# Kernel optimization log

Hardware: AMD Instinct MI355X
Metric: run time of the kernel (lower is better)

Reference implementation:

```python
import jax, jax.numpy as jnp
import numpy as np

DIM = 1024
NUM_HEADS = 16
HEAD_DIM = DIM // NUM_HEADS
SCALE = HEAD_DIM ** -0.5


def setup_inputs() -> dict:
    key = jax.random.key(0)
    ks = jax.random.split(key, 11)
    B, N, M = 8, 1024, 1024
    s = DIM ** -0.5  # init scale for weights
    return {
        "x": jax.random.normal(ks[0], (B, N, DIM), jnp.float32),
        "context": jax.random.normal(ks[1], (B, M, DIM), jnp.float32),
        "Wq": jax.random.normal(ks[2], (DIM, DIM), jnp.float32) * s,
        "bq": jax.random.normal(ks[3], (DIM,), jnp.float32) * 0.01,
        "Wk": jax.random.normal(ks[4], (DIM, DIM), jnp.float32) * s,
        "bk": jax.random.normal(ks[5], (DIM,), jnp.float32) * 0.01,
        "Wv": jax.random.normal(ks[6], (DIM, DIM), jnp.float32) * s,
        "bv": jax.random.normal(ks[7], (DIM,), jnp.float32) * 0.01,
        "Wo": jax.random.normal(ks[8], (DIM, DIM), jnp.float32) * s,
        "bo": jax.random.normal(ks[9], (DIM,), jnp.float32) * 0.01,
    }


def reference(x, context, Wq, bq, Wk, bk, Wv, bv, Wo, bo):
    B, N, _ = x.shape
    M = context.shape[1]
    # Linear projections (torch Linear: x @ W.T + b; here W stored as [in, out])
    q = x @ Wq + bq            # [B, N, DIM]
    k = context @ Wk + bk      # [B, M, DIM]
    v = context @ Wv + bv      # [B, M, DIM]
    # split heads: b n (h d) -> b h n d
    q = q.reshape(B, N, NUM_HEADS, HEAD_DIM).transpose(0, 2, 1, 3)
    k = k.reshape(B, M, NUM_HEADS, HEAD_DIM).transpose(0, 2, 1, 3)
    v = v.reshape(B, M, NUM_HEADS, HEAD_DIM).transpose(0, 2, 1, 3)
    dots = jnp.einsum('bhnd,bhmd->bhnm', q, k) * SCALE
    attn = jax.nn.softmax(dots, axis=-1)
    out = jnp.einsum('bhnm,bhmd->bhnd', attn, v)   # [B, H, N, d]
    out = out.transpose(0, 2, 1, 3).reshape(B, N, DIM)  # b h n d -> b n (h d)
    return out @ Wo + bo
```

## Files before the change

### kernel.cpp

```cpp
#include <hip/hip_runtime.h>

typedef unsigned short u16;
typedef __attribute__((ext_vector_type(8))) short bf16x8;
typedef __attribute__((ext_vector_type(4))) float f32x4;
typedef __attribute__((ext_vector_type(16))) float f32x16;
typedef __attribute__((ext_vector_type(4))) unsigned u32x4;

#define MFMA16 __builtin_amdgcn_mfma_f32_16x16x32_bf16
#define MFMA32 __builtin_amdgcn_mfma_f32_32x32x16_bf16

__device__ __forceinline__ u16 f2b(float f) {
  unsigned u = __builtin_bit_cast(unsigned, f);
  u = (u + 0x7fffu + ((u >> 16) & 1u)) >> 16;
  return (u16)u;
}

__device__ __forceinline__ void gload_lds16(const u16* g, u16* l) {
  __builtin_amdgcn_global_load_lds((const __attribute__((address_space(1))) void*)g,
                                   (__attribute__((address_space(3))) void*)l, 16, 0, 0);
}

__global__ void cvt_bf16(const float* __restrict__ a, const float* __restrict__ b,
                         u16* __restrict__ oa, u16* __restrict__ ob, int n4) {
  int i = blockIdx.x * blockDim.x + threadIdx.x;
  if (i >= n4) return;
  const float* in = blockIdx.z ? b : a;
  u16* out = blockIdx.z ? ob : oa;
  float4 v = reinterpret_cast<const float4*>(in)[i];
  ushort4 o = make_ushort4(f2b(v.x), f2b(v.y), f2b(v.z), f2b(v.w));
  reinterpret_cast<ushort4*>(out)[i] = o;
}

__global__ void wtrans(const float* __restrict__ w0, const float* __restrict__ w1,
                       const float* __restrict__ w2, const float* __restrict__ w3,
                       u16* __restrict__ o0, u16* __restrict__ o1,
                       u16* __restrict__ o2, u16* __restrict__ o3) {
  const float* src = blockIdx.z == 0 ? w0 : blockIdx.z == 1 ? w1 : blockIdx.z == 2 ? w2 : w3;
  u16* dst = blockIdx.z == 0 ? o0 : blockIdx.z == 1 ? o1 : blockIdx.z == 2 ? o2 : o3;
  __shared__ float t[64][65];
  const int tid = threadIdx.x;
  const int r0 = blockIdx.y * 64, c0 = blockIdx.x * 64;
  #pragma unroll
  for (int it = 0; it < 4; ++it) {
    int row = it * 16 + (tid >> 4);
    int col = (tid & 15) * 4;
    float4 v = *reinterpret_cast<const float4*>(&src[(size_t)(r0 + row) * 1024 + c0 + col]);
    t[row][col] = v.x; t[row][col + 1] = v.y; t[row][col + 2] = v.z; t[row][col + 3] = v.w;
  }
  __syncthreads();
  #pragma unroll
  for (int it = 0; it < 2; ++it) {
    int c = it * 32 + (tid >> 3);
    int r8 = (tid & 7) * 8;
    u16 tmp[8];
    #pragma unroll
    for (int k = 0; k < 8; ++k) tmp[k] = f2b(t[r8 + k][c]);
    uint4 pk;
    pk.x = (unsigned)tmp[0] | ((unsigned)tmp[1] << 16);
    pk.y = (unsigned)tmp[2] | ((unsigned)tmp[3] << 16);
    pk.z = (unsigned)tmp[4] | ((unsigned)tmp[5] << 16);
    pk.w = (unsigned)tmp[6] | ((unsigned)tmp[7] << 16);
    *reinterpret_cast<uint4*>(&dst[(size_t)(c0 + c) * 1024 + r0 + r8]) = pk;
  }
}

__device__ __forceinline__ void gemm_core(const u16* __restrict__ A, const u16* __restrict__ Wt,
                                          f32x4 (&acc)[4][4], int brow, int bcol,
                                          u16* __restrict__ smem) {
  const int tid = threadIdx.x;
  const int lane = tid & 63;
  const int w = tid >> 6;
  const int wr = w >> 1, wc = w & 1;
  const int l16 = lane & 15, g = lane >> 4;

  auto stage = [&](int buf, int kt) {
    #pragma unroll
    for (int it = 0; it < 4; ++it) {
      int c = it * 256 + tid;
      int row = (c >> 2) & 127;
      int ks = c >> 9;
      int k8 = c & 3;
      const size_t gofs = (size_t)kt * 64 + ks * 32 + k8 * 8;
      gload_lds16(&A[(size_t)(brow + row) * 1024 + gofs],
                  &smem[buf * 8192 + (it * 256 + w * 64) * 8]);
      gload_lds16(&Wt[(size_t)(bcol + row) * 1024 + gofs],
                  &smem[16384 + buf * 8192 + (it * 256 + w * 64) * 8]);
    }
  };

  stage(0, 0);
  __syncthreads();
  int cur = 0;
  for (int kt = 0; kt < 16; ++kt) {
    if (kt < 15) stage(cur ^ 1, kt + 1);
    const u16* As = &smem[cur * 8192];
    const u16* Bs = &smem[16384 + cur * 8192];
    #pragma unroll
    for (int ks = 0; ks < 2; ++ks) {
      bf16x8 a[4], b[4];
      const int kb = ks * 4096 + g * 8;
      #pragma unroll
      for (int mi = 0; mi < 4; ++mi)
        a[mi] = *reinterpret_cast<const bf16x8*>(&As[kb + (wr * 64 + mi * 16 + l16) * 32]);
      #pragma unroll
      for (int ni = 0; ni < 4; ++ni)
        b[ni] = *reinterpret_cast<const bf16x8*>(&Bs[kb + (wc * 64 + ni * 16 + l16) * 32]);
      #pragma unroll
      for (int mi = 0; mi < 4; ++mi)
        #pragma unroll
        for (int ni = 0; ni < 4; ++ni)
          acc[mi][ni] = MFMA16(a[mi], b[ni], acc[mi][ni], 0, 0, 0);
    }
    __syncthreads();
    cur ^= 1;
  }
}

__global__ __launch_bounds__(256, 2) void gemm_qkv(const u16* __restrict__ xb, const u16* __restrict__ cb,
                                                   const u16* __restrict__ Wqt, const u16* __restrict__ Wkt,
                                                   const u16* __restrict__ Wvt,
                                                   const float* __restrict__ bq, const float* __restrict__ bk,
                                                   const float* __restrict__ bv,
                                                   u16* __restrict__ Qb, u16* __restrict__ Kb,
                                                   u16* __restrict__ Vt) {
  __shared__ u16 smem[32768];
  const int z = blockIdx.z;
  const u16* A = z == 0 ? xb : cb;
  const u16* W = z == 0 ? Wqt : z == 1 ? Wkt : Wvt;
  const float* bias = z == 0 ? bq : z == 1 ? bk : bv;
  const int brow = blockIdx.x * 128, bcol = blockIdx.y * 128;
  f32x4 acc[4][4] = {};
  gemm_core(A, W, acc, brow, bcol, smem);

  const int lane = threadIdx.x & 63;
  const int w = threadIdx.x >> 6;
  const int wr = w >> 1, wc = w & 1;
  const int l16 = lane & 15, g = lane >> 4;
  const float CS = 0.125f * 1.44269504089f;

  if (z < 2) {
    u16* o = z == 0 ? Qb : Kb;
    #pragma unroll
    for (int ni = 0; ni < 4; ++ni) {
      const int col = bcol + wc * 64 + ni * 16 + l16;
      const float bz = bias[col];
      #pragma unroll
      for (int mi = 0; mi < 4; ++mi) {
        const int r0 = brow + wr * 64 + mi * 16 + g * 4;
        f32x4 v = acc[mi][ni];
        #pragma unroll
        for (int j = 0; j < 4; ++j) {
          float val = v[j] + bz;
          if (z == 0) val *= CS;
          o[(size_t)(r0 + j) * 1024 + col] = f2b(val);
        }
      }
    }
  } else {
    u16* T = &smem[w * 4608];
    #pragma unroll
    for (int ni = 0; ni < 4; ++ni) {
      const int col = bcol + wc * 64 + ni * 16 + l16;
      const float bz = bias[col];
      #pragma unroll
      for (int mi = 0; mi < 4; ++mi) {
        f32x4 v = acc[mi][ni];
        #pragma unroll
        for (int j = 0; j < 4; ++j)
          T[(ni * 16 + l16) * 72 + mi * 16 + g * 4 + j] = f2b(v[j] + bz);
      }
    }
    const int h = (bcol + wc * 64) >> 6;
    const int m0 = brow + wr * 64;
    const int bb = m0 >> 10, mloc = m0 & 1023;
    u16* vb = &Vt[((size_t)(bb * 16 + h) * 64) * 1024 + mloc];
    #pragma unroll
    for (int it = 0; it < 8; ++it) {
      const int d = it * 8 + (lane >> 3);
      const int m8 = (lane & 7) * 8;
      bf16x8 val = *reinterpret_cast<const bf16x8*>(&T[d * 72 + m8]);
      *reinterpret_cast<bf16x8*>(&vb[(size_t)d * 1024 + m8]) = val;
    }
  }
}

__global__ __launch_bounds__(256, 2) void gemm_o(const u16* __restrict__ A, const u16* __restrict__ Wt,
                                                 const float* __restrict__ bias, float* __restrict__ outp) {
  __shared__ u16 smem[32768];
  const int brow = blockIdx.x * 128, bcol = blockIdx.y * 128;
  f32x4 acc[4][4] = {};
  gemm_core(A, Wt, acc, brow, bcol, smem);
  const int lane = threadIdx.x & 63;
  const int w = threadIdx.x >> 6;
  const int wr = w >> 1, wc = w & 1;
  const int l16 = lane & 15, g = lane >> 4;
  #pragma unroll
  for (int ni = 0; ni < 4; ++ni) {
    const int col = bcol + wc * 64 + ni * 16 + l16;
    const float bz = bias[col];
    #pragma unroll
    for (int mi = 0; mi < 4; ++mi) {
      const int r0 = brow + wr * 64 + mi * 16 + g * 4;
      f32x4 v = acc[mi][ni];
      #pragma unroll
      for (int j = 0; j < 4; ++j) outp[(size_t)(r0 + j) * 1024 + col] = v[j] + bz;
    }
  }
}

__global__ __launch_bounds__(256, 2) void attn2(const u16* __restrict__ Q, const u16* __restrict__ K,
                                                const u16* __restrict__ Vt, u16* __restrict__ AO) {
  __shared__ u16 Ks[2][64 * 64];
  __shared__ u16 Vs[2][64 * 64];
  const int tid = threadIdx.x, lane = tid & 63, w = tid >> 6;
  const int l32 = lane & 31, u = lane >> 5;
  const int id = blockIdx.x;
  const int v = (id & 7) * 128 + (id >> 3);
  const int qt = v & 7, h = (v >> 3) & 15, b = v >> 7;
  const int q0 = qt * 128 + w * 32;
  const int sw = l32 & 7;

  bf16x8 qf[4];
  {
    const u16* qp = &Q[(size_t)(b * 1024 + q0 + l32) * 1024 + h * 64 + u * 8];
    #pragma unroll
    for (int m = 0; m < 4; ++m) qf[m] = *reinterpret_cast<const bf16x8*>(qp + m * 16);
  }

  f32x16 o0 = {}, o1 = {};
  float lr = 0.f;

  const u16* Kg = K + (size_t)(b * 1024) * 1024 + h * 64;
  const u16* Vg = Vt + (size_t)(b * 16 + h) * 64 * 1024;

  auto stage = [&](int buf, int kt) {
    #pragma unroll
    for (int i = 0; i < 2; ++i) {
      int c = w * 128 + i * 64 + lane;
      int r = c >> 3;
      int gc = ((c & 7) ^ (r & 7)) * 8;
      gload_lds16(&Kg[(size_t)(kt * 64 + r) * 1024 + gc], &Ks[buf][(w * 128 + i * 64) * 8]);
      gload_lds16(&Vg[(size_t)r * 1024 + kt * 64 + gc], &Vs[buf][(w * 128 + i * 64) * 8]);
    }
  };

  stage(0, 0);
  __syncthreads();
  int cur = 0;

  for (int kt = 0; kt < 16; ++kt) {
    if (kt < 15) stage(cur ^ 1, kt + 1);

    f32x16 s0 = {}, s1 = {};
    __builtin_amdgcn_s_setprio(1);
    #pragma unroll
    for (int m = 0; m < 4; ++m) {
      bf16x8 k0 = *reinterpret_cast<const bf16x8*>(&Ks[cur][(size_t)l32 * 64 + (((2 * m + u) ^ sw) * 8)]);
      bf16x8 k1 = *reinterpret_cast<const bf16x8*>(&Ks[cur][(size_t)(32 + l32) * 64 + (((2 * m + u) ^ sw) * 8)]);
      s0 = MFMA32(k0, qf[m], s0, 0, 0, 0);
      s1 = MFMA32(k1, qf[m], s1, 0, 0, 0);
    }
    __builtin_amdgcn_s_setprio(0);

    unsigned W0[8], W1[8];
    #pragma unroll
    for (int j = 0; j < 8; ++j) {
      const int r = 4 * (j >> 1) + 2 * (j & 1);
      float pa0 = __builtin_amdgcn_exp2f(s0[r]);
      float pb0 = __builtin_amdgcn_exp2f(s0[r + 1]);
      float pa1 = __builtin_amdgcn_exp2f(s1[r]);
      float pb1 = __builtin_amdgcn_exp2f(s1[r + 1]);
      lr += (pa0 + pb0) + (pa1 + pb1);
      asm("v_cvt_pk_bf16_f32 %0, %1, %2" : "=v"(W0[j]) : "v"(pa0), "v"(pb0));
      asm("v_cvt_pk_bf16_f32 %0, %1, %2" : "=v"(W1[j]) : "v"(pa1), "v"(pb1));
    }

    unsigned paw[4][4];
    #pragma unroll
    for (int ks = 0; ks < 4; ++ks) {
      const int ksl = ks & 1;
      #pragma unroll
      for (int p = 0; p < 2; ++p) {
        unsigned x = (ks < 2) ? W0[4 * ksl + p] : W1[4 * ksl + p];
        unsigned y = (ks < 2) ? W0[4 * ksl + 2 + p] : W1[4 * ksl + 2 + p];
        asm("v_permlane32_swap_b32 %0, %1" : "+v"(x), "+v"(y));
        paw[ks][p] = x;
        paw[ks][2 + p] = y;
      }
    }

    __builtin_amdgcn_s_setprio(1);
    #pragma unroll
    for (int ks = 0; ks < 4; ++ks) {
      bf16x8 pa = __builtin_bit_cast(bf16x8, u32x4{paw[ks][0], paw[ks][1], paw[ks][2], paw[ks][3]});
      bf16x8 v0 = *reinterpret_cast<const bf16x8*>(&Vs[cur][(size_t)l32 * 64 + (((2 * ks + u) ^ sw) * 8)]);
      bf16x8 v1 = *reinterpret_cast<const bf16x8*>(&Vs[cur][(size_t)(32 + l32) * 64 + (((2 * ks + u) ^ sw) * 8)]);
      o0 = MFMA32(pa, v0, o0, 0, 0, 0);
      o1 = MFMA32(pa, v1, o1, 0, 0, 0);
    }
    __builtin_amdgcn_s_setprio(0);

    __syncthreads();
    cur ^= 1;
  }

  float sum = lr + __shfl_xor(lr, 32);
  float rinv = 1.0f / sum;
  u16* aop = &AO[(size_t)(b * 1024 + q0) * 1024 + h * 64 + l32];
  #pragma unroll
  for (int r = 0; r < 16; ++r) {
    const int ql = (r & 3) + 8 * (r >> 2) + 4 * u;
    int ri_i = __builtin_amdgcn_ds_bpermute((ql + (u << 5)) << 2, __builtin_bit_cast(int, rinv));
    float ri = __builtin_bit_cast(float, ri_i);
    aop[(size_t)ql * 1024] = f2b(o0[r] * ri);
    aop[(size_t)ql * 1024 + 32] = f2b(o1[r] * ri);
  }
}

extern "C" void kernel_launch(void* const* d_in, const int* in_sizes, int n_in,
                              void* d_out, int out_size, void* d_ws, size_t ws_size,
                              hipStream_t stream) {
  const float* x   = (const float*)d_in[0];
  const float* ctx = (const float*)d_in[1];
  const float* Wq  = (const float*)d_in[2];
  const float* bq  = (const float*)d_in[3];
  const float* Wk  = (const float*)d_in[4];
  const float* bk  = (const float*)d_in[5];
  const float* Wv  = (const float*)d_in[6];
  const float* bv  = (const float*)d_in[7];
  const float* Wo  = (const float*)d_in[8];
  const float* bo  = (const float*)d_in[9];
  float* out = (float*)d_out;
  char* ws = (char*)d_ws;

  u16* xb  = (u16*)(ws + (size_t)0);
  u16* cb  = (u16*)(ws + ((size_t)16 << 20));
  u16* Qb  = (u16*)(ws + ((size_t)32 << 20));
  u16* Kb  = (u16*)(ws + ((size_t)48 << 20));
  u16* Vt  = (u16*)(ws + ((size_t)64 << 20));
  u16* Wqt = (u16*)(ws + ((size_t)80 << 20));
  u16* Wkt = (u16*)(ws + ((size_t)82 << 20));
  u16* Wvt = (u16*)(ws + ((size_t)84 << 20));
  u16* Wot = (u16*)(ws + ((size_t)86 << 20));

  const int n4 = (8 * 1024 * 1024) / 4;
  cvt_bf16<<<dim3(8192, 1, 2), 256, 0, stream>>>(x, ctx, xb, cb, n4);
  wtrans<<<dim3(16, 16, 4), 256, 0, stream>>>(Wq, Wk, Wv, Wo, Wqt, Wkt, Wvt, Wot);

  gemm_qkv<<<dim3(64, 8, 3), 256, 0, stream>>>(xb, cb, Wqt, Wkt, Wvt, bq, bk, bv, Qb, Kb, Vt);
  attn2<<<dim3(1024), 256, 0, stream>>>(Qb, Kb, Vt, xb );
  gemm_o<<<dim3(64, 8), 256, 0, stream>>>(xb, Wot, bo, out);
}
```

Baseline: 152.4 us.

## Pre-tile K/V into MFMA fragment order and merge prep kernels

The QKV GEMM epilogue now stages results through LDS and writes K and V as contiguous per-(batch,head,64-key) tiles already arranged in MFMA fragment order. Q stores become vectorized 16-byte rows. The attention kernel can then load each tile with contiguous global-to-LDS copies and read fragments with linear, unswizzled LDS addresses. The fp32→bf16 input conversion and weight transpose kernels are merged into one launch, which adds many idle blocks in the weight branch and risks LDS bank conflicts from the new unswizzled reads.

```diff
diff --git a/kernel.cpp b/kernel.cpp
--- a/kernel.cpp
+++ b/kernel.cpp
@@ -20,26 +20,29 @@
                                    (__attribute__((address_space(3))) void*)l, 16, 0, 0);
 }
 
-__global__ void cvt_bf16(const float* __restrict__ a, const float* __restrict__ b,
-                         u16* __restrict__ oa, u16* __restrict__ ob, int n4) {
-  int i = blockIdx.x * blockDim.x + threadIdx.x;
-  if (i >= n4) return;
-  const float* in = blockIdx.z ? b : a;
-  u16* out = blockIdx.z ? ob : oa;
-  float4 v = reinterpret_cast<const float4*>(in)[i];
-  ushort4 o = make_ushort4(f2b(v.x), f2b(v.y), f2b(v.z), f2b(v.w));
-  reinterpret_cast<ushort4*>(out)[i] = o;
-}
-
-__global__ void wtrans(const float* __restrict__ w0, const float* __restrict__ w1,
-                       const float* __restrict__ w2, const float* __restrict__ w3,
-                       u16* __restrict__ o0, u16* __restrict__ o1,
-                       u16* __restrict__ o2, u16* __restrict__ o3) {
-  const float* src = blockIdx.z == 0 ? w0 : blockIdx.z == 1 ? w1 : blockIdx.z == 2 ? w2 : w3;
-  u16* dst = blockIdx.z == 0 ? o0 : blockIdx.z == 1 ? o1 : blockIdx.z == 2 ? o2 : o3;
+__global__ void prep(const float* __restrict__ x, const float* __restrict__ ctx,
+                     u16* __restrict__ xb, u16* __restrict__ cb,
+                     const float* __restrict__ w0, const float* __restrict__ w1,
+                     const float* __restrict__ w2, const float* __restrict__ w3,
+                     u16* __restrict__ o0, u16* __restrict__ o1,
+                     u16* __restrict__ o2, u16* __restrict__ o3) {
   __shared__ float t[64][65];
+  const int z = blockIdx.z;
   const int tid = threadIdx.x;
-  const int r0 = blockIdx.y * 64, c0 = blockIdx.x * 64;
+  if (z < 2) {
+    int i = blockIdx.x * blockDim.x + tid;
+    const float* in = z ? ctx : x;
+    u16* out = z ? cb : xb;
+    float4 v = reinterpret_cast<const float4*>(in)[i];
+    reinterpret_cast<ushort4*>(out)[i] = make_ushort4(f2b(v.x), f2b(v.y), f2b(v.z), f2b(v.w));
+    return;
+  }
+  const int id = blockIdx.x;
+  if (id >= 1024) return;
+  const int wsel = id >> 8;
+  const float* src = wsel == 0 ? w0 : wsel == 1 ? w1 : wsel == 2 ? w2 : w3;
+  u16* dst = wsel == 0 ? o0 : wsel == 1 ? o1 : wsel == 2 ? o2 : o3;
+  const int r0 = ((id >> 4) & 15) * 64, c0 = (id & 15) * 64;
   #pragma unroll
   for (int it = 0; it < 4; ++it) {
     int row = it * 16 + (tid >> 4);
@@ -121,8 +124,8 @@
                                                    const u16* __restrict__ Wvt,
                                                    const float* __restrict__ bq, const float* __restrict__ bk,
                                                    const float* __restrict__ bv,
-                                                   u16* __restrict__ Qb, u16* __restrict__ Kb,
-                                                   u16* __restrict__ Vt) {
+                                                   u16* __restrict__ Qb, u16* __restrict__ Kf,
+                                                   u16* __restrict__ Vf) {
   __shared__ u16 smem[32768];
   const int z = blockIdx.z;
   const u16* A = z == 0 ? xb : cb;
@@ -137,49 +140,71 @@
   const int wr = w >> 1, wc = w & 1;
   const int l16 = lane & 15, g = lane >> 4;
   const float CS = 0.125f * 1.44269504089f;
+  u16* T = &smem[w * 5120];
 
   if (z < 2) {
-    u16* o = z == 0 ? Qb : Kb;
     #pragma unroll
     for (int ni = 0; ni < 4; ++ni) {
-      const int col = bcol + wc * 64 + ni * 16 + l16;
-      const float bz = bias[col];
+      const float bz = bias[bcol + wc * 64 + ni * 16 + l16];
       #pragma unroll
       for (int mi = 0; mi < 4; ++mi) {
-        const int r0 = brow + wr * 64 + mi * 16 + g * 4;
         f32x4 v = acc[mi][ni];
         #pragma unroll
         for (int j = 0; j < 4; ++j) {
           float val = v[j] + bz;
           if (z == 0) val *= CS;
-          o[(size_t)(r0 + j) * 1024 + col] = f2b(val);
+          T[(mi * 16 + g * 4 + j) * 80 + ni * 16 + l16] = f2b(val);
         }
       }
     }
+    const int r0b = brow + wr * 64;
+    const int colb = bcol + wc * 64;
+    if (z == 0) {
+      #pragma unroll
+      for (int it = 0; it < 8; ++it) {
+        const int rl = it * 8 + (lane >> 3);
+        const int c8 = (lane & 7) * 8;
+        bf16x8 val = *reinterpret_cast<const bf16x8*>(&T[rl * 80 + c8]);
+        *reinterpret_cast<bf16x8*>(&Qb[(size_t)(r0b + rl) * 1024 + colb + c8]) = val;
+      }
+    } else {
+      const int h = colb >> 6;
+      const int bb = r0b >> 10;
+      const int kt = (r0b & 1023) >> 6;
+      u16* kb2 = &Kf[(((size_t)(bb * 16 + h)) * 16 + kt) * 4096];
+      #pragma unroll
+      for (int it = 0; it < 8; ++it) {
+        const int rl = it * 8 + (lane >> 3);
+        const int c8 = (lane & 7) * 8;
+        bf16x8 val = *reinterpret_cast<const bf16x8*>(&T[rl * 80 + c8]);
+        const int chunk = (c8 >> 4) * 128 + (rl >> 5) * 64 + ((c8 >> 3) & 1) * 32 + (rl & 31);
+        *reinterpret_cast<bf16x8*>(&kb2[chunk * 8]) = val;
+      }
+    }
   } else {
-    u16* T = &smem[w * 4608];
     #pragma unroll
     for (int ni = 0; ni < 4; ++ni) {
-      const int col = bcol + wc * 64 + ni * 16 + l16;
-      const float bz = bias[col];
+      const float bz = bias[bcol + wc * 64 + ni * 16 + l16];
       #pragma unroll
       for (int mi = 0; mi < 4; ++mi) {
         f32x4 v = acc[mi][ni];
         #pragma unroll
         for (int j = 0; j < 4; ++j)
-          T[(ni * 16 + l16) * 72 + mi * 16 + g * 4 + j] = f2b(v[j] + bz);
+          T[(ni * 16 + l16) * 80 + mi * 16 + g * 4 + j] = f2b(v[j] + bz);
       }
     }
     const int h = (bcol + wc * 64) >> 6;
     const int m0 = brow + wr * 64;
-    const int bb = m0 >> 10, mloc = m0 & 1023;
-    u16* vb = &Vt[((size_t)(bb * 16 + h) * 64) * 1024 + mloc];
+    const int bb = m0 >> 10;
+    const int kt = (m0 & 1023) >> 6;
+    u16* vb = &Vf[(((size_t)(bb * 16 + h)) * 16 + kt) * 4096];
     #pragma unroll
     for (int it = 0; it < 8; ++it) {
       const int d = it * 8 + (lane >> 3);
       const int m8 = (lane & 7) * 8;
-      bf16x8 val = *reinterpret_cast<const bf16x8*>(&T[d * 72 + m8]);
-      *reinterpret_cast<bf16x8*>(&vb[(size_t)d * 1024 + m8]) = val;
+      bf16x8 val = *reinterpret_cast<const bf16x8*>(&T[d * 80 + m8]);
+      const int chunk = (m8 >> 4) * 128 + (d >> 5) * 64 + ((m8 >> 3) & 1) * 32 + (d & 31);
+      *reinterpret_cast<bf16x8*>(&vb[chunk * 8]) = val;
     }
   }
 }
@@ -208,8 +233,8 @@
   }
 }
 
-__global__ __launch_bounds__(256, 2) void attn2(const u16* __restrict__ Q, const u16* __restrict__ K,
-                                                const u16* __restrict__ Vt, u16* __restrict__ AO) {
+__global__ __launch_bounds__(256, 2) void attn2(const u16* __restrict__ Q, const u16* __restrict__ Kf,
+                                                const u16* __restrict__ Vf, u16* __restrict__ AO) {
   __shared__ u16 Ks[2][64 * 64];
   __shared__ u16 Vs[2][64 * 64];
   const int tid = threadIdx.x, lane = tid & 63, w = tid >> 6;
@@ -218,7 +243,6 @@
   const int v = (id & 7) * 128 + (id >> 3);
   const int qt = v & 7, h = (v >> 3) & 15, b = v >> 7;
   const int q0 = qt * 128 + w * 32;
-  const int sw = l32 & 7;
 
   bf16x8 qf[4];
   {
@@ -230,17 +254,15 @@
   f32x16 o0 = {}, o1 = {};
   float lr = 0.f;
 
-  const u16* Kg = K + (size_t)(b * 1024) * 1024 + h * 64;
-  const u16* Vg = Vt + (size_t)(b * 16 + h) * 64 * 1024;
+  const u16* Kbh = Kf + (size_t)(b * 16 + h) * 65536;
+  const u16* Vbh = Vf + (size_t)(b * 16 + h) * 65536;
 
   auto stage = [&](int buf, int kt) {
     #pragma unroll
-    for (int i = 0; i < 2; ++i) {
-      int c = w * 128 + i * 64 + lane;
-      int r = c >> 3;
-      int gc = ((c & 7) ^ (r & 7)) * 8;
-      gload_lds16(&Kg[(size_t)(kt * 64 + r) * 1024 + gc], &Ks[buf][(w * 128 + i * 64) * 8]);
-      gload_lds16(&Vg[(size_t)r * 1024 + kt * 64 + gc], &Vs[buf][(w * 128 + i * 64) * 8]);
+    for (int it = 0; it < 2; ++it) {
+      const int c = (it * 256 + tid) * 8;
+      gload_lds16(&Kbh[kt * 4096 + c], &Ks[buf][(it * 256 + w * 64) * 8]);
+      gload_lds16(&Vbh[kt * 4096 + c], &Vs[buf][(it * 256 + w * 64) * 8]);
     }
   };
 
@@ -255,8 +277,8 @@
     __builtin_amdgcn_s_setprio(1);
     #pragma unroll
     for (int m = 0; m < 4; ++m) {
-      bf16x8 k0 = *reinterpret_cast<const bf16x8*>(&Ks[cur][(size_t)l32 * 64 + (((2 * m + u) ^ sw) * 8)]);
-      bf16x8 k1 = *reinterpret_cast<const bf16x8*>(&Ks[cur][(size_t)(32 + l32) * 64 + (((2 * m + u) ^ sw) * 8)]);
+      bf16x8 k0 = *reinterpret_cast<const bf16x8*>(&Ks[cur][m * 1024 + lane * 8]);
+      bf16x8 k1 = *reinterpret_cast<const bf16x8*>(&Ks[cur][m * 1024 + 512 + lane * 8]);
       s0 = MFMA32(k0, qf[m], s0, 0, 0, 0);
       s1 = MFMA32(k1, qf[m], s1, 0, 0, 0);
     }
@@ -293,8 +315,8 @@
     #pragma unroll
     for (int ks = 0; ks < 4; ++ks) {
       bf16x8 pa = __builtin_bit_cast(bf16x8, u32x4{paw[ks][0], paw[ks][1], paw[ks][2], paw[ks][3]});
-      bf16x8 v0 = *reinterpret_cast<const bf16x8*>(&Vs[cur][(size_t)l32 * 64 + (((2 * ks + u) ^ sw) * 8)]);
-      bf16x8 v1 = *reinterpret_cast<const bf16x8*>(&Vs[cur][(size_t)(32 + l32) * 64 + (((2 * ks + u) ^ sw) * 8)]);
+      bf16x8 v0 = *reinterpret_cast<const bf16x8*>(&Vs[cur][ks * 1024 + lane * 8]);
+      bf16x8 v1 = *reinterpret_cast<const bf16x8*>(&Vs[cur][ks * 1024 + 512 + lane * 8]);
       o0 = MFMA32(pa, v0, o0, 0, 0, 0);
       o1 = MFMA32(pa, v1, o1, 0, 0, 0);
     }
@@ -336,18 +358,15 @@
   u16* xb  = (u16*)(ws + (size_t)0);
   u16* cb  = (u16*)(ws + ((size_t)16 << 20));
   u16* Qb  = (u16*)(ws + ((size_t)32 << 20));
-  u16* Kb  = (u16*)(ws + ((size_t)48 << 20));
-  u16* Vt  = (u16*)(ws + ((size_t)64 << 20));
+  u16* Kf  = (u16*)(ws + ((size_t)48 << 20));
+  u16* Vf  = (u16*)(ws + ((size_t)64 << 20));
   u16* Wqt = (u16*)(ws + ((size_t)80 << 20));
   u16* Wkt = (u16*)(ws + ((size_t)82 << 20));
   u16* Wvt = (u16*)(ws + ((size_t)84 << 20));
   u16* Wot = (u16*)(ws + ((size_t)86 << 20));
 
-  const int n4 = (8 * 1024 * 1024) / 4;
-  cvt_bf16<<<dim3(8192, 1, 2), 256, 0, stream>>>(x, ctx, xb, cb, n4);
-  wtrans<<<dim3(16, 16, 4), 256, 0, stream>>>(Wq, Wk, Wv, Wo, Wqt, Wkt, Wvt, Wot);
-
-  gemm_qkv<<<dim3(64, 8, 3), 256, 0, stream>>>(xb, cb, Wqt, Wkt, Wvt, bq, bk, bv, Qb, Kb, Vt);
-  attn2<<<dim3(1024), 256, 0, stream>>>(Qb, Kb, Vt, xb );
+  prep<<<dim3(8192, 1, 3), 256, 0, stream>>>(x, ctx, xb, cb, Wq, Wk, Wv, Wo, Wqt, Wkt, Wvt, Wot);
+  gemm_qkv<<<dim3(64, 8, 3), 256, 0, stream>>>(xb, cb, Wqt, Wkt, Wvt, bq, bk, bv, Qb, Kf, Vf);
+  attn2<<<dim3(1024), 256, 0, stream>>>(Qb, Kf, Vf, xb );
   gemm_o<<<dim3(64, 8), 256, 0, stream>>>(xb, Wot, bo, out);
 }
```

Result: no change. 152.3 us (-0.1%).
